# Optimization experiments

Measured on AMD Instinct MI355X. Metric: run time of the kernel, lower is better.

Reference implementation:

```python
import jax, jax.numpy as jnp
import numpy as np

N_NODES = 50000
N_EDGES = 800000
IN_DIM = 128
OUT_DIM = 128
NUM_EDGE_TYPES = 16
RULE_FEAT_DIM = 4


def setup_inputs() -> dict:
    key = jax.random.key(0)
    ks = jax.random.split(key, 20)
    d = OUT_DIM
    s_in = 1.0 / np.sqrt(IN_DIM)
    s_d = 1.0 / np.sqrt(d)
    s_r = 1.0 / np.sqrt(RULE_FEAT_DIM)
    inp = {
        "x": jax.random.normal(ks[0], (N_NODES, IN_DIM), jnp.float32),
        "edge_index": jax.random.randint(ks[1], (2, N_EDGES), 0, N_NODES),
        "edge_type": jax.random.randint(ks[2], (N_EDGES,), 0, NUM_EDGE_TYPES),
        "edge_rule_feat": jax.random.normal(ks[3], (N_EDGES, RULE_FEAT_DIM), jnp.float32),
        "total_nodes": N_NODES,
        # parameters (Linear stored as [in, out]; y = x @ W + b)
        "Wq": jax.random.uniform(ks[4], (IN_DIM, d), jnp.float32, -s_in, s_in),
        "bq": jnp.zeros((d,), jnp.float32),
        "Wk": jax.random.uniform(ks[5], (IN_DIM, d), jnp.float32, -s_in, s_in),
        "bk": jnp.zeros((d,), jnp.float32),
        "Wv": jax.random.uniform(ks[6], (IN_DIM, d), jnp.float32, -s_in, s_in),
        "bv": jnp.zeros((d,), jnp.float32),
        "rel_emb": jax.random.normal(ks[7], (NUM_EDGE_TYPES, d), jnp.float32),
        "attn_vec": jax.random.normal(ks[8], (3 * d,), jnp.float32),
        "rule_w1": jax.random.uniform(ks[9], (RULE_FEAT_DIM, d), jnp.float32, -s_r, s_r),
        "rule_b1": jnp.zeros((d,), jnp.float32),
        "rule_w2": jax.random.uniform(ks[10], (d, 1), jnp.float32, -s_d, s_d),
        "rule_b2": jnp.zeros((1,), jnp.float32),  # zero-initialized in source
        "gate_rule_w": jax.random.uniform(ks[11], (RULE_FEAT_DIM, 1), jnp.float32, -s_r, s_r),
        "gate_rule_b": jnp.zeros((1,), jnp.float32),
        "gate_neural_w": jax.random.uniform(ks[12], (2 * d, 1), jnp.float32, -1.0 / np.sqrt(2 * d), 1.0 / np.sqrt(2 * d)),
        "gate_neural_b": jnp.zeros((1,), jnp.float32),
        "msg_w": jax.random.uniform(ks[13], (d, d), jnp.float32, -s_d, s_d),
        "msg_b": jnp.zeros((d,), jnp.float32),
    }
    return inp


def reference(x, edge_index, edge_type, edge_rule_feat, total_nodes,
              Wq, bq, Wk, bk, Wv, bv, rel_emb, attn_vec,
              rule_w1, rule_b1, rule_w2, rule_b2,
              gate_rule_w, gate_rule_b, gate_neural_w, gate_neural_b,
              msg_w, msg_b):
    src, dst = edge_index[0], edge_index[1]
    d = msg_w.shape[0]

    h_src = x[src] @ Wk + bk                  # [E, d]
    h_dst = x[dst] @ Wq + bq                  # [E, d]
    rel = rel_emb[edge_type]                  # [E, d]

    # (cat([h_src,h_dst,rel]) * attn_vec).sum(-1) without materializing the concat
    a1, a2, a3 = attn_vec[:d], attn_vec[d:2 * d], attn_vec[2 * d:]
    e_base = jax.nn.leaky_relu(h_src @ a1 + h_dst @ a2 + rel @ a3, negative_slope=0.2)

    hidden = jax.nn.relu(edge_rule_feat @ rule_w1 + rule_b1)
    b_ij = (hidden @ rule_w2)[:, 0] + rule_b2[0]          # rule bias per edge

    gate_logit = (edge_rule_feat @ gate_rule_w)[:, 0] + gate_rule_b[0] \
               + (h_src @ gate_neural_w[:d, 0] + h_dst @ gate_neural_w[d:, 0]) + gate_neural_b[0]
    gamma_ij = jax.nn.sigmoid(gate_logit)

    e = e_base + gamma_ij * b_ij

    n = total_nodes
    # segment softmax over dst (numerically stable)
    seg_max = jax.ops.segment_max(e, dst, num_segments=n)
    e_exp = jnp.exp(e - seg_max[dst])
    seg_sum = jax.ops.segment_sum(e_exp, dst, num_segments=n)
    alpha = e_exp / (seg_sum[dst] + 1e-16)

    # eval mode: dropout is identity
    msg = ((x[src] @ Wv + bv + rel) @ msg_w + msg_b) * alpha[:, None]
    out = jax.ops.segment_sum(msg, dst, num_segments=n)   # index_add over dst
    return out, alpha, gamma_ij, b_ij
```

## Files before the change

kernel.cpp:

```cpp
#include <hip/hip_runtime.h>
#include <math.h>


__device__ __forceinline__ float wave_max(float v) {
    #pragma unroll
    for (int o = 32; o > 0; o >>= 1) v = fmaxf(v, __shfl_xor(v, o, 64));
    return v;
}
__device__ __forceinline__ float wave_sum(float v) {
    #pragma unroll
    for (int o = 32; o > 0; o >>= 1) v += __shfl_xor(v, o, 64);
    return v;
}

__device__ __forceinline__ unsigned bf16rne(float f) {
    unsigned u = __float_as_uint(f);
    return (u + 0x7FFFu + ((u >> 16) & 1u)) >> 16;
}
__device__ __forceinline__ float bflo(unsigned u) { return __uint_as_float(u << 16); }
__device__ __forceinline__ float bfhi(unsigned u) { return __uint_as_float(u & 0xFFFF0000u); }

__global__ void __launch_bounds__(128) precompute_kernel(
    const float* __restrict__ Wq, const float* __restrict__ bq,
    const float* __restrict__ Wk, const float* __restrict__ bk,
    const float* __restrict__ Wv, const float* __restrict__ bv,
    const float* __restrict__ rel_emb, const float* __restrict__ attn_vec,
    const float* __restrict__ msg_w, const float* __restrict__ msg_b,
    const float* __restrict__ gnw, const float* __restrict__ grb,
    const float* __restrict__ gnb,
    const float* __restrict__ rule_w1, const float* __restrict__ rule_b1,
    const float* __restrict__ rule_w2,
    unsigned short* __restrict__ W2b, float* __restrict__ c2,
    float* __restrict__ wkA, float* __restrict__ wqA,
    float* __restrict__ wkG, float* __restrict__ wqG,
    float* __restrict__ relA, float* __restrict__ relM,
    float* __restrict__ consts,
    float4* __restrict__ w1t, float2* __restrict__ w12)
{
    __shared__ float red[128];
    int bid = blockIdx.x, j = threadIdx.x;

    auto blk_reduce = [&](float v) -> float {
        red[j] = v;
        __syncthreads();
        for (int s = 64; s > 0; s >>= 1) {
            if (j < s) red[j] += red[j + s];
            __syncthreads();
        }
        float r = red[0];
        __syncthreads();
        return r;
    };

    if (bid < 128) {
        int i = bid;
        float acc = 0.f;
        #pragma unroll 8
        for (int k = 0; k < 128; ++k) acc = fmaf(Wv[i * 128 + k], msg_w[k * 128 + j], acc);
        W2b[i * 128 + j] = (unsigned short)bf16rne(acc);
        float r;
        r = blk_reduce(Wk[i * 128 + j] * attn_vec[j]);        if (j == 0) wkA[i] = r;
        r = blk_reduce(Wq[i * 128 + j] * attn_vec[128 + j]);  if (j == 0) wqA[i] = r;
        r = blk_reduce(Wk[i * 128 + j] * gnw[j]);             if (j == 0) wkG[i] = r;
        r = blk_reduce(Wq[i * 128 + j] * gnw[128 + j]);       if (j == 0) wqG[i] = r;
    } else if (bid < 144) {
        int t = bid - 128;
        float acc = 0.f;
        #pragma unroll 8
        for (int k = 0; k < 128; ++k) acc = fmaf(rel_emb[t * 128 + k], msg_w[k * 128 + j], acc);
        relM[t * 128 + j] = acc;
        float r = blk_reduce(rel_emb[t * 128 + j] * attn_vec[256 + j]);
        if (j == 0) relA[t] = r;
    } else if (bid == 144) {
        float acc = msg_b[j];
        #pragma unroll 8
        for (int k = 0; k < 128; ++k) acc = fmaf(bv[k], msg_w[k * 128 + j], acc);
        c2[j] = acc;
        w1t[j] = make_float4(rule_w1[j], rule_w1[128 + j], rule_w1[256 + j], rule_w1[384 + j]);
        w12[j] = make_float2(rule_b1[j], rule_w2[j]);
    } else {
        float r = blk_reduce(bk[j] * attn_vec[j] + bq[j] * attn_vec[128 + j]);
        if (j == 0) consts[0] = r;
        r = blk_reduce(bk[j] * gnw[j] + bq[j] * gnw[128 + j]);
        if (j == 0) consts[1] = r + grb[0] + gnb[0];
    }
}

__global__ void __launch_bounds__(256) node_kernel(
    const float4* __restrict__ x4, const unsigned short* __restrict__ W2b,
    const float* __restrict__ c2,
    const float* __restrict__ wkA, const float* __restrict__ wqA,
    const float* __restrict__ wkG, const float* __restrict__ wqG,
    unsigned* __restrict__ Vmb, float2* __restrict__ srcPack,
    float2* __restrict__ dstPack, int* __restrict__ deg, int n_nodes)
{
    __shared__ unsigned short Asu[128][136];
    __shared__ unsigned short Bsu[128][136];
    const int tid = threadIdx.x;
    const int rowBase = blockIdx.x * 128;

    if (tid < 128 && rowBase + tid < n_nodes) deg[rowBase + tid] = 0;

    #pragma unroll
    for (int l = 0; l < 16; ++l) {
        int flat = l * 256 + tid;
        int k = flat >> 5, n4 = flat & 31;
        uint2 w = *(const uint2*)&W2b[k * 128 + n4 * 4];
        *(uint2*)&Bsu[k][n4 * 4] = w;
    }
    #pragma unroll
    for (int l = 0; l < 16; ++l) {
        int flat = l * 256 + tid;
        int r = flat & 127;
        int k4 = flat >> 7;
        int row = rowBase + r;
        float4 v = (row < n_nodes) ? x4[row * 32 + k4] : make_float4(0.f, 0.f, 0.f, 0.f);
        Asu[4 * k4 + 0][r] = (unsigned short)bf16rne(v.x);
        Asu[4 * k4 + 1][r] = (unsigned short)bf16rne(v.y);
        Asu[4 * k4 + 2][r] = (unsigned short)bf16rne(v.z);
        Asu[4 * k4 + 3][r] = (unsigned short)bf16rne(v.w);
    }

    {
        int r = tid & 127, h = tid >> 7;
        int row = rowBase + r;
        if (row < n_nodes) {
            const float4* wa4 = (const float4*)(h ? wqA : wkA);
            const float4* wg4 = (const float4*)(h ? wqG : wkG);
            float sA = 0.f, sG = 0.f;
            #pragma unroll 8
            for (int k4 = 0; k4 < 32; ++k4) {
                float4 xv = x4[row * 32 + k4];
                float4 wa = wa4[k4], wg = wg4[k4];
                sA = fmaf(xv.x, wa.x, fmaf(xv.y, wa.y, fmaf(xv.z, wa.z, fmaf(xv.w, wa.w, sA))));
                sG = fmaf(xv.x, wg.x, fmaf(xv.y, wg.y, fmaf(xv.z, wg.z, fmaf(xv.w, wg.w, sG))));
            }
            if (h) dstPack[row] = make_float2(sA, sG);
            else   srcPack[row] = make_float2(sA, sG);
        }
    }
    __syncthreads();

    const int tx = tid & 15, ty = tid >> 4;
    float acc[8][8];
    #pragma unroll
    for (int i = 0; i < 8; ++i)
        #pragma unroll
        for (int j = 0; j < 8; ++j) acc[i][j] = 0.f;

    #pragma unroll 2
    for (int k = 0; k < 128; ++k) {
        uint4 au = *(const uint4*)&Asu[k][ty * 8];
        uint4 bu = *(const uint4*)&Bsu[k][tx * 8];
        float a[8] = {bflo(au.x), bfhi(au.x), bflo(au.y), bfhi(au.y),
                      bflo(au.z), bfhi(au.z), bflo(au.w), bfhi(au.w)};
        float b[8] = {bflo(bu.x), bfhi(bu.x), bflo(bu.y), bfhi(bu.y),
                      bflo(bu.z), bfhi(bu.z), bflo(bu.w), bfhi(bu.w)};
        #pragma unroll
        for (int i = 0; i < 8; ++i)
            #pragma unroll
            for (int j = 0; j < 8; ++j)
                acc[i][j] = fmaf(a[i], b[j], acc[i][j]);
    }

    float c2v[8];
    #pragma unroll
    for (int j = 0; j < 8; ++j) c2v[j] = c2[tx * 8 + j];
    #pragma unroll
    for (int i = 0; i < 8; ++i) {
        int row = rowBase + ty * 8 + i;
        if (row < n_nodes) {
            uint4 o;
            o.x = bf16rne(acc[i][0] + c2v[0]) | (bf16rne(acc[i][1] + c2v[1]) << 16);
            o.y = bf16rne(acc[i][2] + c2v[2]) | (bf16rne(acc[i][3] + c2v[3]) << 16);
            o.z = bf16rne(acc[i][4] + c2v[4]) | (bf16rne(acc[i][5] + c2v[5]) << 16);
            o.w = bf16rne(acc[i][6] + c2v[6]) | (bf16rne(acc[i][7] + c2v[7]) << 16);
            *(uint4*)&Vmb[row * 64 + tx * 4] = o;
        }
    }
}

__global__ void __launch_bounds__(256) edge1_kernel(
    const int* __restrict__ ei, const int* __restrict__ et,
    const float4* __restrict__ erf,
    const float4* __restrict__ w1t, const float2* __restrict__ w12,
    const float* __restrict__ rule_b2, const float* __restrict__ grw,
    const float2* __restrict__ srcPack, const float2* __restrict__ dstPack,
    const float* __restrict__ relA, const float* __restrict__ consts,
    float* __restrict__ e_val, float* __restrict__ gamma_out,
    float* __restrict__ b_out, int* __restrict__ deg,
    int n_edges)
{
    __shared__ float4 s_w1t[128];
    __shared__ float2 s_w12[128];
    int tid = threadIdx.x;
    if (tid < 128) { s_w1t[tid] = w1t[tid]; s_w12[tid] = w12[tid]; }
    __syncthreads();
    int e = blockIdx.x * 256 + tid;
    if (e >= n_edges) return;

    int s = ei[e], d = ei[n_edges + e], t = et[e];
    float4 rf = erf[e];
    float2 ss = srcPack[s], dd = dstPack[d];

    float pre = ss.x + dd.x + relA[t] + consts[0];
    float e_base = pre >= 0.f ? pre : 0.2f * pre;

    float b = rule_b2[0];
    #pragma unroll 8
    for (int j = 0; j < 128; ++j) {
        float4 w = s_w1t[j];
        float2 bw = s_w12[j];
        float h = fmaf(rf.x, w.x, fmaf(rf.y, w.y, fmaf(rf.z, w.z, fmaf(rf.w, w.w, bw.x))));
        b = fmaf(fmaxf(h, 0.f), bw.y, b);
    }

    float gl = fmaf(rf.x, grw[0], fmaf(rf.y, grw[1],
               fmaf(rf.z, grw[2], fmaf(rf.w, grw[3], consts[1] + ss.y + dd.y))));
    float gamma = 1.f / (1.f + __expf(-gl));

    gamma_out[e] = gamma;
    b_out[e] = b;
    e_val[e] = e_base + gamma * b;
    atomicAdd(&deg[d], 1);
}

__global__ void __launch_bounds__(256) scan1_kernel(
    const int* __restrict__ deg, int* __restrict__ rowPtr,
    int* __restrict__ partials, int n)
{
    __shared__ int sdata[256];
    int tid = threadIdx.x;
    int base = blockIdx.x * 1024 + tid * 4;
    int v0 = (base + 0 < n) ? deg[base + 0] : 0;
    int v1 = (base + 1 < n) ? deg[base + 1] : 0;
    int v2 = (base + 2 < n) ? deg[base + 2] : 0;
    int v3 = (base + 3 < n) ? deg[base + 3] : 0;
    int tsum = v0 + v1 + v2 + v3;
    sdata[tid] = tsum;
    __syncthreads();
    #pragma unroll
    for (int off = 1; off < 256; off <<= 1) {
        int t = (tid >= off) ? sdata[tid - off] : 0;
        __syncthreads();
        sdata[tid] += t;
        __syncthreads();
    }
    int excl = sdata[tid] - tsum;
    if (base + 0 < n) rowPtr[base + 0] = excl;
    if (base + 1 < n) rowPtr[base + 1] = excl + v0;
    if (base + 2 < n) rowPtr[base + 2] = excl + v0 + v1;
    if (base + 3 < n) rowPtr[base + 3] = excl + v0 + v1 + v2;
    if (tid == 255) partials[blockIdx.x] = sdata[255];
}

__global__ void __launch_bounds__(64) scan2_kernel(int* __restrict__ partials, int nb)
{
    int lane = threadIdx.x;
    int v = (lane < nb) ? partials[lane] : 0;
    int orig = v;
    #pragma unroll
    for (int off = 1; off < 64; off <<= 1) {
        int t = __shfl_up(v, off, 64);
        if (lane >= off) v += t;
    }
    if (lane < nb) partials[lane] = v - orig;
}

__global__ void __launch_bounds__(256) scan3_kernel(
    int* __restrict__ rowPtr, const int* __restrict__ partials,
    int* __restrict__ cursor, int n, int n_edges)
{
    int off = partials[blockIdx.x];
    int base = blockIdx.x * 1024 + threadIdx.x * 4;
    #pragma unroll
    for (int k = 0; k < 4; ++k) {
        int idx = base + k;
        if (idx < n) {
            int r = rowPtr[idx] + off;
            rowPtr[idx] = r;
            cursor[idx] = r;
        }
    }
    if (blockIdx.x == 0 && threadIdx.x == 0) rowPtr[n] = n_edges;
}

__global__ void __launch_bounds__(256) scatter_kernel(
    const int* __restrict__ ei, const int* __restrict__ et,
    const float* __restrict__ e_val, int* __restrict__ cursor,
    float2* __restrict__ payload, int n_edges)
{
    int e = blockIdx.x * blockDim.x + threadIdx.x;
    if (e >= n_edges) return;
    int d = ei[n_edges + e];
    int pos = atomicAdd(&cursor[d], 1);
    int st = ei[e] | (et[e] << 27);
    payload[pos] = make_float2(e_val[e], __int_as_float(st));
}

__global__ void __launch_bounds__(256) gather_kernel(
    const int* __restrict__ rowPtr, const float2* __restrict__ payload,
    const unsigned* __restrict__ Vmb, const float* __restrict__ relM,
    float* __restrict__ out, float2* __restrict__ nodeMS, int n_nodes)
{
    int lane = threadIdx.x & 63;
    int d = blockIdx.x * 4 + (threadIdx.x >> 6);
    if (d >= n_nodes) return;
    int start = rowPtr[d];
    int deg = rowPtr[d + 1] - start;

    float acc0 = 0.f, acc1 = 0.f;
    float m = -INFINITY, inv;

    auto acc4 = [&](float av, int st, int k) {
        float a[4];
        int s[4];
        #pragma unroll
        for (int i = 0; i < 4; ++i) {
            a[i] = __shfl(av, k + i, 64);
            s[i] = __shfl(st, k + i, 64);
        }
        unsigned v[4];
        float2 rm[4];
        #pragma unroll
        for (int i = 0; i < 4; ++i) {
            int ss = s[i] & 0x7FFFFFF;
            int tt = ((unsigned)s[i]) >> 27;
            v[i]  = Vmb[ss * 64 + lane];
            rm[i] = *(const float2*)&relM[tt * 128 + lane * 2];
        }
        #pragma unroll
        for (int i = 0; i < 4; ++i) {
            acc0 = fmaf(a[i], bflo(v[i]) + rm[i].x, acc0);
            acc1 = fmaf(a[i], bfhi(v[i]) + rm[i].y, acc1);
        }
    };

    if (deg <= 64) {
        float ev = -INFINITY;
        int st = 0;
        if (lane < deg) {
            float2 p = payload[start + lane];
            ev = p.x;
            st = __float_as_int(p.y);
        }
        m = wave_max(ev);
        float ex = (lane < deg) ? __expf(ev - m) : 0.f;
        float sum = wave_sum(ex);
        inv = 1.f / (sum + 1e-16f);
        float av = ex * inv;
        for (int k = 0; k < deg; k += 4) acc4(av, st, k);
    } else {
        for (int i = lane; i < deg; i += 64) m = fmaxf(m, payload[start + i].x);
        m = wave_max(m);
        float sum = 0.f;
        for (int i = lane; i < deg; i += 64) sum += __expf(payload[start + i].x - m);
        sum = wave_sum(sum);
        inv = 1.f / (sum + 1e-16f);
        for (int c = 0; c < deg; c += 64) {
            int i = c + lane;
            float av = 0.f;
            int st = 0;
            if (i < deg) {
                float2 p = payload[start + i];
                av = __expf(p.x - m) * inv;
                st = __float_as_int(p.y);
            }
            int cnt = min(64, deg - c);
            for (int k = 0; k < cnt; k += 4) acc4(av, st, k);
        }
    }
    if (lane == 0) nodeMS[d] = make_float2(m, inv);
    *(float2*)&out[d * 128 + lane * 2] = make_float2(acc0, acc1);
}

__global__ void __launch_bounds__(256) alpha_kernel(
    const int* __restrict__ ei, const float* __restrict__ e_val,
    const float2* __restrict__ nodeMS, float* __restrict__ alpha_out, int n_edges)
{
    int e = blockIdx.x * blockDim.x + threadIdx.x;
    if (e >= n_edges) return;
    int d = ei[n_edges + e];
    float2 ms = nodeMS[d];
    alpha_out[e] = __expf(e_val[e] - ms.x) * ms.y;
}

extern "C" void kernel_launch(void* const* d_in, const int* in_sizes, int n_in,
                              void* d_out, int out_size, void* d_ws, size_t ws_size,
                              hipStream_t stream)
{
    const float* x        = (const float*)d_in[0];
    const int*   ei       = (const int*)d_in[1];
    const int*   et       = (const int*)d_in[2];
    const float* erf      = (const float*)d_in[3];
    const float* Wq       = (const float*)d_in[5];
    const float* bq       = (const float*)d_in[6];
    const float* Wk       = (const float*)d_in[7];
    const float* bk       = (const float*)d_in[8];
    const float* Wv       = (const float*)d_in[9];
    const float* bv       = (const float*)d_in[10];
    const float* rel_emb  = (const float*)d_in[11];
    const float* attn_vec = (const float*)d_in[12];
    const float* rule_w1  = (const float*)d_in[13];
    const float* rule_b1  = (const float*)d_in[14];
    const float* rule_w2  = (const float*)d_in[15];
    const float* rule_b2  = (const float*)d_in[16];
    const float* grw      = (const float*)d_in[17];
    const float* grb      = (const float*)d_in[18];
    const float* gnw      = (const float*)d_in[19];
    const float* gnb      = (const float*)d_in[20];
    const float* msg_w    = (const float*)d_in[21];
    const float* msg_b    = (const float*)d_in[22];

    const int n_nodes = in_sizes[0] / 128;
    const int n_edges = in_sizes[2];
    const int nb = (n_nodes + 1023) / 1024;

    float* ws = (float*)d_ws;
    size_t off = 0;
    unsigned* Vmb  = (unsigned*)(ws + off); off += (size_t)n_nodes * 64;
    float2* payload = (float2*)(ws + off); off += 2 * (size_t)n_edges;
    float* e_val   = ws + off; off += n_edges;
    float* srcPack = ws + off; off += 2 * (size_t)n_nodes;
    float* dstPack = ws + off; off += 2 * (size_t)n_nodes;
    float2* nodeMS = (float2*)(ws + off); off += 2 * (size_t)n_nodes;
    int*   deg     = (int*)(ws + off); off += n_nodes;
    int*   rowPtr  = (int*)(ws + off); off += n_nodes + 4;
    int*   partials= (int*)(ws + off); off += 64;
    unsigned short* W2b = (unsigned short*)(ws + off); off += 128 * 64;
    float* c2      = ws + off; off += 128;
    float* wkA     = ws + off; off += 128;
    float* wqA     = ws + off; off += 128;
    float* wkG     = ws + off; off += 128;
    float* wqG     = ws + off; off += 128;
    float* relA    = ws + off; off += 16;
    float* relM    = ws + off; off += 16 * 128;
    float* consts  = ws + off; off += 2;
    off += 2;
    float4* w1t    = (float4*)(ws + off); off += 128 * 4;
    float2* w12    = (float2*)(ws + off); off += 128 * 2;

    float* out       = (float*)d_out;
    float* alpha_out = out + (size_t)n_nodes * 128;
    float* gamma_out = alpha_out + n_edges;
    float* b_out     = gamma_out + n_edges;

    hipLaunchKernelGGL(precompute_kernel, dim3(146), dim3(128), 0, stream,
                       Wq, bq, Wk, bk, Wv, bv, rel_emb, attn_vec, msg_w, msg_b,
                       gnw, grb, gnb, rule_w1, rule_b1, rule_w2,
                       W2b, c2, wkA, wqA, wkG, wqG, relA, relM, consts, w1t, w12);

    hipLaunchKernelGGL(node_kernel, dim3((n_nodes + 127) / 128), dim3(256), 0, stream,
                       (const float4*)x, W2b, c2,
                       wkA, wqA, wkG, wqG, Vmb, (float2*)srcPack, (float2*)dstPack,
                       deg, n_nodes);

    hipLaunchKernelGGL(edge1_kernel, dim3((n_edges + 255) / 256), dim3(256), 0, stream,
                       ei, et, (const float4*)erf, (const float4*)w1t, (const float2*)w12,
                       rule_b2, grw, (const float2*)srcPack, (const float2*)dstPack,
                       relA, consts, e_val, gamma_out, b_out, deg, n_edges);

    hipLaunchKernelGGL(scan1_kernel, dim3(nb), dim3(256), 0, stream,
                       deg, rowPtr, partials, n_nodes);
    hipLaunchKernelGGL(scan2_kernel, dim3(1), dim3(64), 0, stream,
                       partials, nb);
    hipLaunchKernelGGL(scan3_kernel, dim3(nb), dim3(256), 0, stream,
                       rowPtr, partials, deg , n_nodes, n_edges);

    hipLaunchKernelGGL(scatter_kernel, dim3((n_edges + 255) / 256), dim3(256), 0, stream,
                       ei, et, e_val, deg , payload, n_edges);

    hipLaunchKernelGGL(gather_kernel, dim3((n_nodes + 3) / 4), dim3(256), 0, stream,
                       rowPtr, payload, Vmb, relM, out, nodeMS, n_nodes);

    hipLaunchKernelGGL(alpha_kernel, dim3((n_edges + 255) / 256), dim3(256), 0, stream,
                       ei, e_val, nodeMS, alpha_out, n_edges);
}
```

Baseline: 325.5 us.

## Replace atomic scatter with two-pass bucketed counting sort by destination

The per-edge global atomic scatter into CSR order is replaced by a two-level sort. A first pass bins 4096 edges per block into 256-node buckets in shared memory and writes them out contiguously. A second pass then places each edge at its final slot using shared-memory atomics per bucket. This is meant to cut random global atomics and scattered writes, at the cost of an extra temp buffer and one more pass over the edges. The packing assumes src fits in 16 bits (caps at 65536 nodes) and at most 256 buckets.

```diff
diff --git a/kernel.cpp b/kernel.cpp
--- a/kernel.cpp
+++ b/kernel.cpp
@@ -269,7 +269,7 @@
 
 __global__ void __launch_bounds__(256) scan3_kernel(
     int* __restrict__ rowPtr, const int* __restrict__ partials,
-    int* __restrict__ cursor, int n, int n_edges)
+    int* __restrict__ bucketCursor, int n, int n_edges)
 {
     int off = partials[blockIdx.x];
     int base = blockIdx.x * 1024 + threadIdx.x * 4;
@@ -279,23 +279,98 @@
         if (idx < n) {
             int r = rowPtr[idx] + off;
             rowPtr[idx] = r;
-            cursor[idx] = r;
+            if ((idx & 255) == 0) bucketCursor[idx >> 8] = r;
         }
     }
     if (blockIdx.x == 0 && threadIdx.x == 0) rowPtr[n] = n_edges;
 }
 
-__global__ void __launch_bounds__(256) scatter_kernel(
+__global__ void __launch_bounds__(256) sort1_kernel(
     const int* __restrict__ ei, const int* __restrict__ et,
-    const float* __restrict__ e_val, int* __restrict__ cursor,
-    float2* __restrict__ payload, int n_edges)
-{
-    int e = blockIdx.x * blockDim.x + threadIdx.x;
-    if (e >= n_edges) return;
-    int d = ei[n_edges + e];
-    int pos = atomicAdd(&cursor[d], 1);
-    int st = ei[e] | (et[e] << 27);
-    payload[pos] = make_float2(e_val[e], __int_as_float(st));
+    const float* __restrict__ e_val, int* __restrict__ bucketCursor,
+    float2* __restrict__ tmp, int n_edges)
+{
+    __shared__ float2 data[4096];
+    __shared__ unsigned char slotB[4096];
+    __shared__ int cnt[256], rk[256], base_[256], run[256], scanBuf[256];
+    const int tid = threadIdx.x;
+    const int blockBase = blockIdx.x * 4096;
+    const int total = min(4096, n_edges - blockBase);
+
+    cnt[tid] = 0;
+    rk[tid] = 0;
+    __syncthreads();
+
+    int   d_[16];
+    float ev_[16];
+    int   pk_[16];
+    #pragma unroll
+    for (int i = 0; i < 16; ++i) {
+        int e = blockBase + i * 256 + tid;
+        if (e < n_edges) {
+            int d = ei[n_edges + e];
+            d_[i]  = d;
+            ev_[i] = e_val[e];
+            pk_[i] = (ei[e] & 0xFFFF) | ((et[e] & 15) << 16) | ((d & 255) << 20);
+            atomicAdd(&cnt[d >> 8], 1);
+        } else {
+            d_[i] = -1;
+        }
+    }
+    __syncthreads();
+
+    int c = cnt[tid];
+    scanBuf[tid] = c;
+    __syncthreads();
+    #pragma unroll
+    for (int off = 1; off < 256; off <<= 1) {
+        int t = (tid >= off) ? scanBuf[tid - off] : 0;
+        __syncthreads();
+        scanBuf[tid] += t;
+        __syncthreads();
+    }
+    base_[tid] = scanBuf[tid] - c;
+    run[tid] = c ? atomicAdd(&bucketCursor[tid], c) : 0;
+    __syncthreads();
+
+    #pragma unroll
+    for (int i = 0; i < 16; ++i) {
+        if (d_[i] >= 0) {
+            int b = d_[i] >> 8;
+            int r = atomicAdd(&rk[b], 1);
+            int slot = base_[b] + r;
+            data[slot] = make_float2(ev_[i], __int_as_float(pk_[i]));
+            slotB[slot] = (unsigned char)b;
+        }
+    }
+    __syncthreads();
+
+    for (int j = tid; j < total; j += 256) {
+        int b = slotB[j];
+        tmp[run[b] + (j - base_[b])] = data[j];
+    }
+}
+
+__global__ void __launch_bounds__(256) sort2_kernel(
+    const int* __restrict__ rowPtr, const float2* __restrict__ tmp,
+    float2* __restrict__ payload, int n_nodes)
+{
+    __shared__ int cur[256];
+    const int tid = threadIdx.x;
+    const int d0 = blockIdx.x * 256;
+    const int dEnd = min(d0 + 256, n_nodes);
+    if (d0 + tid < dEnd) cur[tid] = rowPtr[d0 + tid];
+    __syncthreads();
+    const int lo = rowPtr[d0];
+    const int hi = rowPtr[dEnd];
+    for (int j = lo + tid; j < hi; j += 256) {
+        float2 p = tmp[j];
+        unsigned pk = __float_as_uint(p.y);
+        int dl = (pk >> 20) & 255;
+        int pos = atomicAdd(&cur[dl], 1);
+        unsigned st = (pk & 0xFFFFu) | (((pk >> 16) & 15u) << 27);
+        payload[pos] = make_float2(p.x, __uint_as_float(st));
+    }
 }
 
 __global__ void __launch_bounds__(256) gather_kernel(
@@ -415,11 +490,13 @@
     const int n_nodes = in_sizes[0] / 128;
     const int n_edges = in_sizes[2];
     const int nb = (n_nodes + 1023) / 1024;
+    const int nbuck = (n_nodes + 255) / 256;
 
     float* ws = (float*)d_ws;
     size_t off = 0;
     unsigned* Vmb  = (unsigned*)(ws + off); off += (size_t)n_nodes * 64;
     float2* payload = (float2*)(ws + off); off += 2 * (size_t)n_edges;
+    float2* tmpPay  = (float2*)(ws + off); off += 2 * (size_t)n_edges;
     float* e_val   = ws + off; off += n_edges;
     float* srcPack = ws + off; off += 2 * (size_t)n_nodes;
     float* dstPack = ws + off; off += 2 * (size_t)n_nodes;
@@ -427,6 +504,7 @@
     int*   deg     = (int*)(ws + off); off += n_nodes;
     int*   rowPtr  = (int*)(ws + off); off += n_nodes + 4;
     int*   partials= (int*)(ws + off); off += 64;
+    int*   bucketCursor = (int*)(ws + off); off += 256;
     unsigned short* W2b = (unsigned short*)(ws + off); off += 128 * 64;
     float* c2      = ws + off; off += 128;
     float* wkA     = ws + off; off += 128;
@@ -465,10 +543,13 @@
     hipLaunchKernelGGL(scan2_kernel, dim3(1), dim3(64), 0, stream,
                        partials, nb);
     hipLaunchKernelGGL(scan3_kernel, dim3(nb), dim3(256), 0, stream,
-                       rowPtr, partials, deg , n_nodes, n_edges);
-
-    hipLaunchKernelGGL(scatter_kernel, dim3((n_edges + 255) / 256), dim3(256), 0, stream,
-                       ei, et, e_val, deg , payload, n_edges);
+                       rowPtr, partials, bucketCursor, n_nodes, n_edges);
+
+    hipLaunchKernelGGL(sort1_kernel, dim3((n_edges + 4095) / 4096), dim3(256), 0, stream,
+                       ei, et, e_val, bucketCursor, tmpPay, n_edges);
+
+    hipLaunchKernelGGL(sort2_kernel, dim3(nbuck), dim3(256), 0, stream,
+                       rowPtr, tmpPay, payload, n_nodes);
 
     hipLaunchKernelGGL(gather_kernel, dim3((n_nodes + 3) / 4), dim3(256), 0, stream,
                        rowPtr, payload, Vmb, relM, out, nodeMS, n_nodes);
```

Measured after the change: 296.0 us. 9.0% less time.
